# Kernel optimization log

Measured on AMD Instinct MI355X. Metric: run time of the kernel, lower is better.

The kernel has to match this reference:

```python
import jax, jax.numpy as jnp
import numpy as np

N_HEAD = 16
N_KV = 4
N_EMBD = 2048
HEAD_DIM = N_EMBD // N_HEAD  # 128
GROUP = N_HEAD // N_KV       # 4 queries per kv head


def setup_inputs() -> dict:
    key = jax.random.key(0)
    ks = jax.random.split(key, 5)
    B, S = 2, 2048
    scale = 0.02
    return {
        "x": jax.random.normal(ks[0], (B, S, N_EMBD), dtype=jnp.float32),
        "Wq": jax.random.normal(ks[1], (N_EMBD, N_EMBD), dtype=jnp.float32) * scale,
        "Wk": jax.random.normal(ks[2], (N_EMBD, N_EMBD // GROUP), dtype=jnp.float32) * scale,
        "Wv": jax.random.normal(ks[3], (N_EMBD, N_EMBD // GROUP), dtype=jnp.float32) * scale,
        "Wo": jax.random.normal(ks[4], (N_EMBD, N_EMBD), dtype=jnp.float32) * scale,
    }


def reference(x, Wq, Wk, Wv, Wo):
    B, S, _ = x.shape
    scale = HEAD_DIM ** -0.5
    # projections (bias=False)
    q = (x @ Wq).reshape(B, S, N_KV, GROUP, HEAD_DIM)   # grouped query heads
    k = (x @ Wk).reshape(B, S, N_KV, HEAD_DIM)
    v = (x @ Wv).reshape(B, S, N_KV, HEAD_DIM)
    # scores: repeat_interleave of K over GROUP == broadcast over g axis
    scores = jnp.einsum('bqkgd,bskd->bkgqs', q, k) * scale  # [B,n_kv,g,S,S]
    causal = jnp.triu(jnp.ones((S, S), dtype=bool), k=1)
    scores = jnp.where(causal, jnp.finfo(scores.dtype).min, scores)
    attn = jax.nn.softmax(scores, axis=-1)
    out = jnp.einsum('bkgqs,bskd->bqkgd', attn, v)  # [B,S,n_kv,g,hd]
    out = out.reshape(B, S, N_EMBD)
    return out @ Wo
```

## Files before the change

### kernel.cpp

```cpp
#include <hip/hip_runtime.h>

typedef unsigned short u16;
typedef unsigned int u32;
typedef __attribute__((ext_vector_type(8))) __bf16 bh8;
typedef __attribute__((ext_vector_type(4))) float fx4;

#define AS1 __attribute__((address_space(1)))
#define AS3 __attribute__((address_space(3)))

__device__ __forceinline__ void gll16(const void* g, void* l) {
  void* gg = const_cast<void*>(g);
  __builtin_amdgcn_global_load_lds((AS1 void*)gg, (AS3 void*)l, 16, 0, 0);
}

__device__ __forceinline__ u16 f2b(float f) {
  union { float f; u32 u; } v; v.f = f;
  u32 r = v.u + 0x7FFFu + ((v.u >> 16) & 1u);
  return (u16)(r >> 16);
}

__device__ __forceinline__ fx4 fzero() { fx4 z = {0.f, 0.f, 0.f, 0.f}; return z; }

#define MFMA16(a, b, c) __builtin_amdgcn_mfma_f32_16x16x32_bf16(a, b, c, 0, 0, 0)

__global__ void k_cast(const float* __restrict__ in, u16* __restrict__ out, int n4) {
  int i = blockIdx.x * blockDim.x + threadIdx.x;
  if (i >= n4) return;
  float4 v = reinterpret_cast<const float4*>(in)[i];
  ushort4 o;
  o.x = f2b(v.x); o.y = f2b(v.y); o.z = f2b(v.z); o.w = f2b(v.w);
  reinterpret_cast<ushort4*>(out)[i] = o;
}

__global__ void k_transpose_cast(const float* __restrict__ in, u16* __restrict__ out,
                                 int R, int C) {
  __shared__ float t[32][33];
  int tx = threadIdx.x, ty = threadIdx.y;
  int r0 = blockIdx.y * 32, c0 = blockIdx.x * 32;
#pragma unroll
  for (int j = 0; j < 4; j++)
    t[ty + 8 * j][tx] = in[(size_t)(r0 + ty + 8 * j) * C + c0 + tx];
  __syncthreads();
#pragma unroll
  for (int j = 0; j < 4; j++)
    out[(size_t)(c0 + ty + 8 * j) * R + r0 + tx] = f2b(t[tx][ty + 8 * j]);
}

__global__ void k_transpose_v(const u16* __restrict__ in, u16* __restrict__ out) {
  __shared__ u16 t[32][33];
  int tx = threadIdx.x, ty = threadIdx.y;
  int s0 = blockIdx.x * 32, d0 = blockIdx.y * 32;
  int z = blockIdx.z, b = z >> 2, kv = z & 3;
#pragma unroll
  for (int j = 0; j < 4; j++)
    t[ty + 8 * j][tx] = in[(size_t)(b * 2048 + s0 + ty + 8 * j) * 512 + kv * 128 + d0 + tx];
  __syncthreads();
#pragma unroll
  for (int j = 0; j < 4; j++)
    out[(size_t)(z * 128 + d0 + ty + 8 * j) * 2048 + s0 + tx] = t[tx][ty + 8 * j];
}

__device__ __forceinline__ void gemm_core(const u16* __restrict__ A, const u16* __restrict__ Bt,
                                          int bm, int bn, u16* As, u16* Bs, fx4 acc[4][4]) {
  const int tid = threadIdx.x;
  const int lane = tid & 63, w = tid >> 6;
  const int wr = w >> 1, wc = w & 1;
  const int i = lane & 15, g = lane >> 4;
  const int c0 = tid, c1 = tid + 256;
  const u16* ga0 = A + (size_t)(bm + (c0 >> 2)) * 2048 + (c0 & 3) * 8;
  const u16* ga1 = A + (size_t)(bm + (c1 >> 2)) * 2048 + (c1 & 3) * 8;
  const u16* gb0 = Bt + (size_t)(bn + (c0 >> 2)) * 2048 + (c0 & 3) * 8;
  const u16* gb1 = Bt + (size_t)(bn + (c1 >> 2)) * 2048 + (c1 & 3) * 8;
  u16* la0 = As + c0 * 8; u16* la1 = As + c1 * 8;
  u16* lb0 = Bs + c0 * 8; u16* lb1 = Bs + c1 * 8;
  const u16* ra = As + (wr * 64 + i) * 32 + g * 8;
  const u16* rb = Bs + (wc * 64 + i) * 32 + g * 8;
  for (int kt = 0; kt < 2048; kt += 32) {
    __syncthreads();
    gll16(ga0 + kt, la0);
    gll16(ga1 + kt, la1);
    gll16(gb0 + kt, lb0);
    gll16(gb1 + kt, lb1);
    __syncthreads();
    bh8 af[4], bfr[4];
#pragma unroll
    for (int m = 0; m < 4; m++) af[m] = *reinterpret_cast<const bh8*>(ra + m * 16 * 32);
#pragma unroll
    for (int n = 0; n < 4; n++) bfr[n] = *reinterpret_cast<const bh8*>(rb + n * 16 * 32);
#pragma unroll
    for (int m = 0; m < 4; m++)
#pragma unroll
      for (int n = 0; n < 4; n++)
        acc[m][n] = MFMA16(af[m], bfr[n], acc[m][n]);
  }
}

__global__ __launch_bounds__(256, 2) void k_proj(const u16* __restrict__ xb,
                                                 const u16* __restrict__ Wqt,
                                                 const u16* __restrict__ Wkt,
                                                 const u16* __restrict__ Wvt,
                                                 u16* __restrict__ Qb, u16* __restrict__ Kb,
                                                 u16* __restrict__ Vb) {
  __shared__ __align__(16) u16 As[128 * 32];
  __shared__ __align__(16) u16 Bs[128 * 32];
  int by = blockIdx.y;
  const u16* Bt; u16* Cp; int bn, ldc; float alpha;
  if (by < 16)      { Bt = Wqt; Cp = Qb; bn = by * 128;        ldc = 2048; alpha = 0.08838834764831845f; }
  else if (by < 20) { Bt = Wkt; Cp = Kb; bn = (by - 16) * 128; ldc = 512;  alpha = 1.0f; }
  else              { Bt = Wvt; Cp = Vb; bn = (by - 20) * 128; ldc = 512;  alpha = 1.0f; }
  int bm = blockIdx.x * 128;
  fx4 acc[4][4];
#pragma unroll
  for (int m = 0; m < 4; m++)
#pragma unroll
    for (int n = 0; n < 4; n++) acc[m][n] = fzero();
  gemm_core(xb, Bt, bm, bn, As, Bs, acc);
  const int lane = threadIdx.x & 63, w = threadIdx.x >> 6;
  const int wr = w >> 1, wc = w & 1, i = lane & 15, g = lane >> 4;
#pragma unroll
  for (int m = 0; m < 4; m++)
#pragma unroll
    for (int n = 0; n < 4; n++)
#pragma unroll
      for (int r = 0; r < 4; r++) {
        int row = bm + wr * 64 + m * 16 + 4 * g + r;
        int col = bn + wc * 64 + n * 16 + i;
        Cp[(size_t)row * ldc + col] = f2b(acc[m][n][r] * alpha);
      }
}

__global__ __launch_bounds__(256, 2) void k_gemm_out(const u16* __restrict__ Ob,
                                                     const u16* __restrict__ Wot,
                                                     float* __restrict__ C) {
  __shared__ __align__(16) u16 As[128 * 32];
  __shared__ __align__(16) u16 Bs[128 * 32];
  int bm = blockIdx.x * 128, bn = blockIdx.y * 128;
  fx4 acc[4][4];
#pragma unroll
  for (int m = 0; m < 4; m++)
#pragma unroll
    for (int n = 0; n < 4; n++) acc[m][n] = fzero();
  gemm_core(Ob, Wot, bm, bn, As, Bs, acc);
  const int lane = threadIdx.x & 63, w = threadIdx.x >> 6;
  const int wr = w >> 1, wc = w & 1, i = lane & 15, g = lane >> 4;
#pragma unroll
  for (int m = 0; m < 4; m++)
#pragma unroll
    for (int n = 0; n < 4; n++)
#pragma unroll
      for (int r = 0; r < 4; r++) {
        int row = bm + wr * 64 + m * 16 + 4 * g + r;
        int col = bn + wc * 64 + n * 16 + i;
        C[(size_t)row * 2048 + col] = acc[m][n][r];
      }
}

__global__ __launch_bounds__(512, 4) void k_attn(const u16* __restrict__ Qb,
                                                 const u16* __restrict__ Kb,
                                                 const u16* __restrict__ Vt,
                                                 u16* __restrict__ Ob) {
  __shared__ __align__(16) u16 Ks0[64 * 128], Ks1[64 * 128];
  __shared__ __align__(16) u16 Vs0[128 * 64], Vs1[128 * 64];
  __shared__ __align__(16) u16 Pl[8][16 * 64];
  const int tid = threadIdx.x, lane = tid & 63, w = tid >> 6;
  const int i = lane & 15, g = lane >> 4;
  const int j = blockIdx.x;
  const int head = blockIdx.y, b = blockIdx.z, kv = head >> 2;
  const bool isA = (w >= 4);
  const int qt = isA ? j : (31 - j);
  const int qmin = qt * 64 + (w & 3) * 16;
  const int nt = 32 - j;
  const int myNt = isA ? (j + 1) : nt;

  const u16* Kbb = Kb + (size_t)b * 2048 * 512 + kv * 128;
  const u16* Vbb = Vt + (size_t)(b * 4 + kv) * 128 * 2048;

  bh8 qf[4];
  {
    const u16* qp = Qb + (size_t)(b * 2048 + qmin + i) * 2048 + head * 128 + g * 8;
#pragma unroll
    for (int kb = 0; kb < 4; kb++) qf[kb] = *reinterpret_cast<const bh8*>(qp + kb * 32);
  }

  fx4 o[8];
#pragma unroll
  for (int dt = 0; dt < 8; dt++) o[dt] = fzero();
  float m[4] = {-1e30f, -1e30f, -1e30f, -1e30f};
  float l[4] = {0.f, 0.f, 0.f, 0.f};

  auto STAGE = [&](u16* Kd, u16* Vd, int s0) {
#pragma unroll
    for (int cc = 0; cc < 2; cc++) {
      int c = tid + cc * 512;
      gll16(Kbb + (size_t)(s0 + (c >> 4)) * 512 + (((c & 15) ^ ((c >> 4) & 7)) * 8),
            Kd + c * 8);
      gll16(Vbb + (size_t)(c >> 3) * 2048 + s0 + (((c & 7) ^ ((c >> 3) & 7)) * 8),
            Vd + c * 8);
    }
  };

  auto TILE = [&](const u16* Kbuf, const u16* Vbuf, int s0) {
    fx4 sc[4];
#pragma unroll
    for (int st = 0; st < 4; st++) {
      sc[st] = fzero();
#pragma unroll
      for (int kb = 0; kb < 4; kb++) {
        bh8 kf = *reinterpret_cast<const bh8*>(Kbuf + (st * 16 + i) * 128 +
                                               (((kb * 4 + g) ^ (i & 7)) * 8));
        sc[st] = MFMA16(qf[kb], kf, sc[st]);
      }
    }
    if (s0 + 63 > qmin) {
#pragma unroll
      for (int st = 0; st < 4; st++)
#pragma unroll
        for (int r = 0; r < 4; r++) {
          int s = s0 + st * 16 + i;
          int q = qmin + 4 * g + r;
          if (s > q) sc[st][r] = -1e30f;
        }
    }
    float corr[4];
#pragma unroll
    for (int r = 0; r < 4; r++) {
      float v = fmaxf(fmaxf(sc[0][r], sc[1][r]), fmaxf(sc[2][r], sc[3][r]));
      v = fmaxf(v, __shfl_xor(v, 1));
      v = fmaxf(v, __shfl_xor(v, 2));
      v = fmaxf(v, __shfl_xor(v, 4));
      v = fmaxf(v, __shfl_xor(v, 8));
      float mn = fmaxf(m[r], v);
      corr[r] = __expf(m[r] - mn);
      m[r] = mn;
    }
    float p[4][4];
#pragma unroll
    for (int r = 0; r < 4; r++) {
      float s = 0.f;
#pragma unroll
      for (int st = 0; st < 4; st++) { p[st][r] = __expf(sc[st][r] - m[r]); s += p[st][r]; }
      s += __shfl_xor(s, 1); s += __shfl_xor(s, 2);
      s += __shfl_xor(s, 4); s += __shfl_xor(s, 8);
      l[r] = l[r] * corr[r] + s;
    }
#pragma unroll
    for (int dt = 0; dt < 8; dt++)
#pragma unroll
      for (int r = 0; r < 4; r++) o[dt][r] *= corr[r];

#pragma unroll
    for (int st = 0; st < 4; st++)
#pragma unroll
      for (int r = 0; r < 4; r++) {
        int row = 4 * g + r;
        int cg = st * 2 + (i >> 3);
        Pl[w][row * 64 + ((cg ^ (row & 7)) << 3) + (i & 7)] = f2b(p[st][r]);
      }
    bh8 pf0 = *reinterpret_cast<const bh8*>(&Pl[w][i * 64 + ((g ^ (i & 7)) << 3)]);
    bh8 pf1 = *reinterpret_cast<const bh8*>(&Pl[w][i * 64 + (((4 + g) ^ (i & 7)) << 3)]);
#pragma unroll
    for (int dt = 0; dt < 8; dt++) {
      bh8 v0 = *reinterpret_cast<const bh8*>(Vbuf + (dt * 16 + i) * 64 +
                                             ((g ^ (i & 7)) * 8));
      bh8 v1 = *reinterpret_cast<const bh8*>(Vbuf + (dt * 16 + i) * 64 +
                                             (((4 + g) ^ (i & 7)) * 8));
      o[dt] = MFMA16(pf0, v0, o[dt]);
      o[dt] = MFMA16(pf1, v1, o[dt]);
    }
  };

  STAGE(Ks0, Vs0, 0);
  __syncthreads();
  for (int t = 0; t < nt; t += 2) {
    if (t + 1 < nt) STAGE(Ks1, Vs1, (t + 1) * 64);
    if (t < myNt) TILE(Ks0, Vs0, t * 64);
    __syncthreads();
    if (t + 1 >= nt) break;
    if (t + 2 < nt) STAGE(Ks0, Vs0, (t + 2) * 64);
    if (t + 1 < myNt) TILE(Ks1, Vs1, (t + 1) * 64);
    __syncthreads();
  }

#pragma unroll
  for (int r = 0; r < 4; r++) {
    float inv = 1.0f / l[r];
#pragma unroll
    for (int dt = 0; dt < 8; dt++)
      Ob[(size_t)(b * 2048 + qmin + 4 * g + r) * 2048 + head * 128 + dt * 16 + i] =
          f2b(o[dt][r] * inv);
  }
}

extern "C" void kernel_launch(void* const* d_in, const int* in_sizes, int n_in,
                              void* d_out, int out_size, void* d_ws, size_t ws_size,
                              hipStream_t stream) {
  (void)in_sizes; (void)n_in; (void)out_size; (void)ws_size;
  const float* x  = (const float*)d_in[0];
  const float* Wq = (const float*)d_in[1];
  const float* Wk = (const float*)d_in[2];
  const float* Wv = (const float*)d_in[3];
  const float* Wo = (const float*)d_in[4];

  char* ws = (char*)d_ws;
  size_t off = 0;
  auto alloc = [&](size_t bytes) {
    void* p = ws + off;
    off += (bytes + 255) & ~(size_t)255;
    return p;
  };
  u16* xb  = (u16*)alloc(8388608ull * 2);
  u16* Wqt = (u16*)alloc(4194304ull * 2);
  u16* Wkt = (u16*)alloc(1048576ull * 2);
  u16* Wvt = (u16*)alloc(1048576ull * 2);
  u16* Wot = (u16*)alloc(4194304ull * 2);
  u16* Qb  = (u16*)alloc(8388608ull * 2);
  u16* Kb  = (u16*)alloc(2097152ull * 2);
  u16* Vb  = (u16*)alloc(2097152ull * 2);
  u16* Vt  = (u16*)alloc(2097152ull * 2);
  u16* Ob  = xb;

  k_cast<<<8192, 256, 0, stream>>>(x, xb, 2097152);
  k_transpose_cast<<<dim3(64, 64), dim3(32, 8), 0, stream>>>(Wq, Wqt, 2048, 2048);
  k_transpose_cast<<<dim3(16, 64), dim3(32, 8), 0, stream>>>(Wk, Wkt, 2048, 512);
  k_transpose_cast<<<dim3(16, 64), dim3(32, 8), 0, stream>>>(Wv, Wvt, 2048, 512);
  k_transpose_cast<<<dim3(64, 64), dim3(32, 8), 0, stream>>>(Wo, Wot, 2048, 2048);
  k_proj<<<dim3(32, 24), 256, 0, stream>>>(xb, Wqt, Wkt, Wvt, Qb, Kb, Vb);
  k_transpose_v<<<dim3(64, 4, 8), dim3(32, 8), 0, stream>>>(Vb, Vt);
  k_attn<<<dim3(16, 16, 2), 512, 0, stream>>>(Qb, Kb, Vt, Ob);
  k_gemm_out<<<dim3(32, 16), 256, 0, stream>>>(Ob, Wot, (float*)d_out);
}
```

Measured before the change: 343.4 us.

## Use lazy softmax rescaling, deferred row-sum reduction, MFMA priority and occupancy bounds

New measurement: 330.0 us. 1.04x faster.

```diff
diff --git a/kernel.cpp b/kernel.cpp
--- a/kernel.cpp
+++ b/kernel.cpp
@@ -95,7 +95,7 @@
   }
 }
 
-__global__ __launch_bounds__(256, 2) void k_proj(const u16* __restrict__ xb,
+__global__ __launch_bounds__(256, 3) void k_proj(const u16* __restrict__ xb,
                                                  const u16* __restrict__ Wqt,
                                                  const u16* __restrict__ Wkt,
                                                  const u16* __restrict__ Wvt,
@@ -129,7 +129,7 @@
       }
 }
 
-__global__ __launch_bounds__(256, 2) void k_gemm_out(const u16* __restrict__ Ob,
+__global__ __launch_bounds__(256, 3) void k_gemm_out(const u16* __restrict__ Ob,
                                                      const u16* __restrict__ Wot,
                                                      float* __restrict__ C) {
   __shared__ __align__(16) u16 As[128 * 32];
@@ -186,7 +186,7 @@
 #pragma unroll
   for (int dt = 0; dt < 8; dt++) o[dt] = fzero();
   float m[4] = {-1e30f, -1e30f, -1e30f, -1e30f};
-  float l[4] = {0.f, 0.f, 0.f, 0.f};
+  float lp[4] = {0.f, 0.f, 0.f, 0.f};
 
   auto STAGE = [&](u16* Kd, u16* Vd, int s0) {
 #pragma unroll
@@ -201,6 +201,7 @@
 
   auto TILE = [&](const u16* Kbuf, const u16* Vbuf, int s0) {
     fx4 sc[4];
+    __builtin_amdgcn_s_setprio(1);
 #pragma unroll
     for (int st = 0; st < 4; st++) {
       sc[st] = fzero();
@@ -211,6 +212,7 @@
         sc[st] = MFMA16(qf[kb], kf, sc[st]);
       }
     }
+    __builtin_amdgcn_s_setprio(0);
     if (s0 + 63 > qmin) {
 #pragma unroll
       for (int st = 0; st < 4; st++)
@@ -221,7 +223,7 @@
           if (s > q) sc[st][r] = -1e30f;
         }
     }
-    float corr[4];
+    float pmax[4];
 #pragma unroll
     for (int r = 0; r < 4; r++) {
       float v = fmaxf(fmaxf(sc[0][r], sc[1][r]), fmaxf(sc[2][r], sc[3][r]));
@@ -229,24 +231,29 @@
       v = fmaxf(v, __shfl_xor(v, 2));
       v = fmaxf(v, __shfl_xor(v, 4));
       v = fmaxf(v, __shfl_xor(v, 8));
-      float mn = fmaxf(m[r], v);
-      corr[r] = __expf(m[r] - mn);
-      m[r] = mn;
+      pmax[r] = v;
+    }
+    int need = 0;
+#pragma unroll
+    for (int r = 0; r < 4; r++) need |= (pmax[r] > m[r] + 8.0f) ? 1 : 0;
+    if (__any(need)) {
+#pragma unroll
+      for (int r = 0; r < 4; r++) {
+        float mn = fmaxf(m[r], pmax[r]);
+        float corr = __expf(m[r] - mn);
+        m[r] = mn;
+        lp[r] *= corr;
+#pragma unroll
+        for (int dt = 0; dt < 8; dt++) o[dt][r] *= corr;
+      }
     }
     float p[4][4];
 #pragma unroll
     for (int r = 0; r < 4; r++) {
-      float s = 0.f;
-#pragma unroll
-      for (int st = 0; st < 4; st++) { p[st][r] = __expf(sc[st][r] - m[r]); s += p[st][r]; }
-      s += __shfl_xor(s, 1); s += __shfl_xor(s, 2);
-      s += __shfl_xor(s, 4); s += __shfl_xor(s, 8);
-      l[r] = l[r] * corr[r] + s;
-    }
-#pragma unroll
-    for (int dt = 0; dt < 8; dt++)
-#pragma unroll
-      for (int r = 0; r < 4; r++) o[dt][r] *= corr[r];
+#pragma unroll
+      for (int st = 0; st < 4; st++) p[st][r] = __expf(sc[st][r] - m[r]);
+      lp[r] += (p[0][r] + p[1][r]) + (p[2][r] + p[3][r]);
+    }
 
 #pragma unroll
     for (int st = 0; st < 4; st++)
@@ -258,6 +265,7 @@
       }
     bh8 pf0 = *reinterpret_cast<const bh8*>(&Pl[w][i * 64 + ((g ^ (i & 7)) << 3)]);
     bh8 pf1 = *reinterpret_cast<const bh8*>(&Pl[w][i * 64 + (((4 + g) ^ (i & 7)) << 3)]);
+    __builtin_amdgcn_s_setprio(1);
 #pragma unroll
     for (int dt = 0; dt < 8; dt++) {
       bh8 v0 = *reinterpret_cast<const bh8*>(Vbuf + (dt * 16 + i) * 64 +
@@ -267,6 +275,7 @@
       o[dt] = MFMA16(pf0, v0, o[dt]);
       o[dt] = MFMA16(pf1, v1, o[dt]);
     }
+    __builtin_amdgcn_s_setprio(0);
   };
 
   STAGE(Ks0, Vs0, 0);
@@ -283,7 +292,12 @@
 
 #pragma unroll
   for (int r = 0; r < 4; r++) {
-    float inv = 1.0f / l[r];
+    float s = lp[r];
+    s += __shfl_xor(s, 1);
+    s += __shfl_xor(s, 2);
+    s += __shfl_xor(s, 4);
+    s += __shfl_xor(s, 8);
+    float inv = 1.0f / s;
 #pragma unroll
     for (int dt = 0; dt < 8; dt++)
       Ob[(size_t)(b * 2048 + qmin + 4 * g + r) * 2048 + head * 128 + dt * 16 + i] =
```
